# Optimization experiments

Measured on AMD Instinct MI355X. Metric: run time of the kernel, lower is better.

The kernel has to match this reference:

```python
import jax, jax.numpy as jnp
import numpy as np

B = 8        # graphs per batch
VG = 20000   # vertices per graph
K = 128      # eigenvectors per graph
D = 128      # channels (C_inout)
V = B * VG


def setup_inputs() -> dict:
    key = jax.random.key(0)
    kx, km, ke, kv, kt = jax.random.split(key, 5)
    x = jax.random.normal(kx, (V, D), dtype=jnp.float32)
    # lumped (diagonal) mass, positive
    mass = jax.random.uniform(km, (V,), dtype=jnp.float32, minval=0.5, maxval=1.5)
    # per-graph nonnegative eigenvalues, sorted within each graph, stacked to (B*K,)
    evals = jnp.sort(jax.random.uniform(ke, (B, K), dtype=jnp.float32) * 10.0, axis=1).reshape(-1)
    # eigenbasis, roughly mass-orthonormal scale
    evecs = jax.random.normal(kv, (V, K), dtype=jnp.float32) / np.sqrt(VG)
    # learned per-channel diffusion times, positive
    diffusion_time = jax.random.uniform(kt, (D,), dtype=jnp.float32, minval=0.01, maxval=0.2)
    batch = jnp.repeat(jnp.arange(B, dtype=jnp.int32), VG)
    return {"x": x, "mass": mass, "evals": evals, "evecs": evecs,
            "diffusion_time": diffusion_time, "batch": batch, "bs": B}


def reference(x, mass, evals, evecs, diffusion_time, batch, bs):
    Vtot, Dc = x.shape
    neig = evals.shape[0] // bs
    vg = Vtot // bs  # equal-sized graphs -> ragged grouped matmul == batched matmul
    t = jnp.maximum(diffusion_time, 1e-8)  # torch clamp(min=1e-8)
    xb = x.reshape(bs, vg, Dc)            # (B, Vg, D)
    eb = evecs.reshape(bs, vg, neig)      # (B, Vg, K)
    mb = mass.reshape(bs, vg)             # (B, Vg) diagonal mass
    # to_basis: basis^T @ (M x) per graph -> (B, K, D)
    x_spec = jnp.einsum('bvk,bvd->bkd', eb * mb[..., None], xb)
    # spectral diffusion coefficients exp(-lambda * t_c): (B, K, D)
    coefs = jnp.exp(-evals.reshape(bs, neig)[..., None] * t[None, None, :])
    # from_basis: evecs @ (coefs * x_spec) per graph -> (B, Vg, D)
    x_diffuse = jnp.einsum('bvk,bkd->bvd', eb, coefs * x_spec)
    return x_diffuse.reshape(Vtot, Dc)
```

## Files before the change

### kernel.cpp

```cpp
#include <hip/hip_runtime.h>

#define BGR 8
#define VG  20000
#define NK  128
#define ND  128

typedef float f32x4 __attribute__((ext_vector_type(4)));
typedef short bf16x8 __attribute__((ext_vector_type(8)));

__device__ __forceinline__ unsigned cvtpk(float a, float b) {
    unsigned r;
    asm("v_cvt_pk_bf16_f32 %0, %1, %2" : "=v"(r) : "v"(a), "v"(b));
    return r;
}

__device__ __forceinline__ short bf16r(float f) {
    union { float f; unsigned u; } c; c.f = f;
    unsigned r = (c.u + 0x7FFFu + ((c.u >> 16) & 1u)) >> 16;
    return (short)r;
}

#define VC  160
#define S1  40
#define NCH (VG / VC)

__global__ __launch_bounds__(256) void k_spec(const float* __restrict__ x,
                                              const float* __restrict__ mass,
                                              const float* __restrict__ evecs,
                                              float* __restrict__ scr) {
    const int bid   = blockIdx.x;
    const int g     = bid & 7;
    const int chunk = bid >> 3;
    const int v0    = chunk * VC;

    const float* xg = x     + (size_t)g * VG * ND;
    const float* eg = evecs + (size_t)g * VG * NK;
    const float* mg = mass  + (size_t)g * VG;

    __shared__ short Et[NK * S1];
    __shared__ short Xt[ND * S1];

    const int tid = threadIdx.x;
    const int l   = tid & 63;
    const int w   = tid >> 6;
    const int lo  = l & 15, hi = l >> 4;
    const int r0  = (w & 1) * 64, c0 = (w >> 1) * 64;

    const int cc = l;
    const int oc = w;

    float eA[8], eB[8], xA[8], xB[8], mm[8];

    auto loadr = [&](int r) {
        const int vb = v0 + r * 32 + oc * 8;
#pragma unroll
        for (int q = 0; q < 8; ++q) {
            const size_t re = (size_t)(vb + q) * NK;
            const size_t rx = (size_t)(vb + q) * ND;
            eA[q] = eg[re + cc];  eB[q] = eg[re + cc + 64];
            xA[q] = xg[rx + cc];  xB[q] = xg[rx + cc + 64];
            mm[q] = mg[vb + q];
        }
    };

    f32x4 acc[4][4] = {};
    loadr(0);

#pragma unroll
    for (int r = 0; r < VC / 32; ++r) {
        uint4 u;
        u.x = cvtpk(eA[0], eA[1]); u.y = cvtpk(eA[2], eA[3]);
        u.z = cvtpk(eA[4], eA[5]); u.w = cvtpk(eA[6], eA[7]);
        *(uint4*)(Et + cc * S1 + oc * 8) = u;
        u.x = cvtpk(eB[0], eB[1]); u.y = cvtpk(eB[2], eB[3]);
        u.z = cvtpk(eB[4], eB[5]); u.w = cvtpk(eB[6], eB[7]);
        *(uint4*)(Et + (cc + 64) * S1 + oc * 8) = u;
        u.x = cvtpk(xA[0] * mm[0], xA[1] * mm[1]); u.y = cvtpk(xA[2] * mm[2], xA[3] * mm[3]);
        u.z = cvtpk(xA[4] * mm[4], xA[5] * mm[5]); u.w = cvtpk(xA[6] * mm[6], xA[7] * mm[7]);
        *(uint4*)(Xt + cc * S1 + oc * 8) = u;
        u.x = cvtpk(xB[0] * mm[0], xB[1] * mm[1]); u.y = cvtpk(xB[2] * mm[2], xB[3] * mm[3]);
        u.z = cvtpk(xB[4] * mm[4], xB[5] * mm[5]); u.w = cvtpk(xB[6] * mm[6], xB[7] * mm[7]);
        *(uint4*)(Xt + (cc + 64) * S1 + oc * 8) = u;

        if (r + 1 < VC / 32) loadr(r + 1);
        __syncthreads();

        bf16x8 ax[4], be[4];
#pragma unroll
        for (int i = 0; i < 4; ++i)
            ax[i] = *(const bf16x8*)(Xt + (r0 + 16 * i + lo) * S1 + hi * 8);
#pragma unroll
        for (int j = 0; j < 4; ++j)
            be[j] = *(const bf16x8*)(Et + (c0 + 16 * j + lo) * S1 + hi * 8);
#pragma unroll
        for (int i = 0; i < 4; ++i)
#pragma unroll
            for (int j = 0; j < 4; ++j)
                acc[i][j] = __builtin_amdgcn_mfma_f32_16x16x32_bf16(ax[i], be[j], acc[i][j], 0, 0, 0);
        __syncthreads();
    }

    float* sg = scr + (size_t)bid * ND * NK;
#pragma unroll
    for (int i = 0; i < 4; ++i)
#pragma unroll
        for (int j = 0; j < 4; ++j)
#pragma unroll
            for (int t = 0; t < 4; ++t) {
                const int dd = r0 + 16 * i + hi * 4 + t;
                const int kk = c0 + 16 * j + lo;
                sg[dd * NK + kk] = acc[i][j][t];
            }
}

__global__ __launch_bounds__(256) void k_coef(const float* __restrict__ scr,
                                              const float* __restrict__ evals,
                                              const float* __restrict__ dt,
                                              short* __restrict__ Yt) {
    const int q   = blockIdx.x * 256 + threadIdx.x;
    const int g   = q >> 14;
    const int rem = q & 16383;
    const int d   = rem >> 7;
    const int k   = rem & 127;
    const float* p = scr + (size_t)g * ND * NK + rem;
    float s = 0.f;
#pragma unroll 25
    for (int c = 0; c < NCH; ++c)
        s += p[(size_t)c * 8 * ND * NK];
    const float t = fmaxf(dt[d], 1e-8f);
    Yt[q] = bf16r(__expf(-evals[g * NK + k] * t) * s);
}

#define TV  64
#define NT  ((VG + TV - 1) / TV)
#define NSL 64

__global__ __launch_bounds__(256) void k_out(const float* __restrict__ evecs,
                                             const short* __restrict__ Yt,
                                             float* __restrict__ out) {
    const int bid  = blockIdx.x;
    const int g    = bid & 7;
    const int slot = bid >> 3;

    const float* eg = evecs + (size_t)g * VG * NK;
    float*       og = out   + (size_t)g * VG * ND;
    const short* yg = Yt    + (size_t)g * ND * NK;

    __shared__ short Bs[128 * 128];
    __shared__ short As[2][TV * 128];

    const int tid = threadIdx.x;

#pragma unroll
    for (int it = 0; it < 8; ++it) {
        const int s16 = it * 256 + tid;
        const int rr  = s16 >> 4, gq = s16 & 15;
        *(uint4*)(Bs + rr * 128 + ((gq ^ (rr & 7)) << 3)) =
            *(const uint4*)(yg + s16 * 8);
    }

    const int vrow = tid >> 2;
    const int q4   = tid & 3;

    float4 ld[8];
    auto load_tile = [&](int t) {
        const int tv0  = t * TV;
        const int rows = (VG - tv0 < TV) ? (VG - tv0) : TV;
        const int vc   = vrow < rows ? vrow : rows - 1;
        const float* src = eg + (size_t)(tv0 + vc) * NK + q4 * 32;
#pragma unroll
        for (int f = 0; f < 8; ++f) ld[f] = *(const float4*)(src + 4 * f);
    };
    auto write_tile = [&](int buf) {
        short* A = As[buf];
#pragma unroll
        for (int h = 0; h < 4; ++h) {
            uint4 u;
            u.x = cvtpk(ld[2 * h].x, ld[2 * h].y);
            u.y = cvtpk(ld[2 * h].z, ld[2 * h].w);
            u.z = cvtpk(ld[2 * h + 1].x, ld[2 * h + 1].y);
            u.w = cvtpk(ld[2 * h + 1].z, ld[2 * h + 1].w);
            const int g8 = q4 * 4 + h;
            *(uint4*)(A + vrow * 128 + ((g8 ^ (vrow & 7)) << 3)) = u;
        }
    };

    const int l  = tid & 63;
    const int w  = tid >> 6;
    const int lo = l & 15, hi = l >> 4;
    const int r0 = (w & 1) * 32, c0 = (w >> 1) * 64;

    int t = slot;
    load_tile(t);
    write_tile(0);
    int cur = 0;

    for (; t < NT; t += NSL) {
        const int tn = t + NSL;
        if (tn < NT) load_tile(tn);
        __syncthreads();

        f32x4 acc[2][4] = {};
        const short* A = As[cur];
#pragma unroll
        for (int ks = 0; ks < 4; ++ks) {
            bf16x8 af[2], bv[4];
#pragma unroll
            for (int i = 0; i < 2; ++i) {
                const int R = r0 + 16 * i + lo;
                af[i] = *(const bf16x8*)(A + R * 128 + ((((ks << 2) + hi) ^ (R & 7)) << 3));
            }
#pragma unroll
            for (int j = 0; j < 4; ++j) {
                const int Dd = c0 + 16 * j + lo;
                bv[j] = *(const bf16x8*)(Bs + Dd * 128 + ((((ks << 2) + hi) ^ (Dd & 7)) << 3));
            }
#pragma unroll
            for (int i = 0; i < 2; ++i)
#pragma unroll
                for (int j = 0; j < 4; ++j)
                    acc[i][j] = __builtin_amdgcn_mfma_f32_16x16x32_bf16(af[i], bv[j], acc[i][j], 0, 0, 0);
        }

        const int tv0  = t * TV;
        const int rows = (VG - tv0 < TV) ? (VG - tv0) : TV;
#pragma unroll
        for (int i = 0; i < 2; ++i)
#pragma unroll
            for (int j = 0; j < 4; ++j)
#pragma unroll
                for (int u = 0; u < 4; ++u) {
                    const int vv = r0 + 16 * i + hi * 4 + u;
                    if (vv < rows)
                        og[(size_t)(tv0 + vv) * ND + c0 + 16 * j + lo] = acc[i][j][u];
                }

        if (tn < NT) write_tile(cur ^ 1);
        cur ^= 1;
    }
}

extern "C" void kernel_launch(void* const* d_in, const int* in_sizes, int n_in,
                              void* d_out, int out_size, void* d_ws, size_t ws_size,
                              hipStream_t stream) {
    const float* x     = (const float*)d_in[0];
    const float* mass  = (const float*)d_in[1];
    const float* evals = (const float*)d_in[2];
    const float* evecs = (const float*)d_in[3];
    const float* dt    = (const float*)d_in[4];
    float* out = (float*)d_out;

    float* scr = out;
    short* Yt  = (short*)d_ws;

    k_spec<<<NCH * BGR, 256, 0, stream>>>(x, mass, evecs, scr);
    k_coef<<<(BGR * ND * NK) / 256, 256, 0, stream>>>(scr, evals, dt, Yt);
    k_out<<<NSL * BGR, 256, 0, stream>>>(evecs, Yt, out);
}
```

Baseline: 252.4 us.

## Deepen load pipelining in spec and output kernels, widen loads, swizzle LDS

```diff
diff --git a/kernel.cpp b/kernel.cpp
--- a/kernel.cpp
+++ b/kernel.cpp
@@ -39,66 +39,80 @@
 
     __shared__ short Et[NK * S1];
     __shared__ short Xt[ND * S1];
+    __shared__ float Ms[VC];
 
     const int tid = threadIdx.x;
     const int l   = tid & 63;
     const int w   = tid >> 6;
     const int lo  = l & 15, hi = l >> 4;
     const int r0  = (w & 1) * 64, c0 = (w >> 1) * 64;
-
-    const int cc = l;
-    const int oc = w;
-
-    float eA[8], eB[8], xA[8], xB[8], mm[8];
-
-    auto loadr = [&](int r) {
-        const int vb = v0 + r * 32 + oc * 8;
-#pragma unroll
-        for (int q = 0; q < 8; ++q) {
-            const size_t re = (size_t)(vb + q) * NK;
-            const size_t rx = (size_t)(vb + q) * ND;
-            eA[q] = eg[re + cc];  eB[q] = eg[re + cc + 64];
-            xA[q] = xg[rx + cc];  xB[q] = xg[rx + cc + 64];
-            mm[q] = mg[vb + q];
-        }
-    };
+    const int oc  = w;
+    const int C0  = 2 * l;
+    const int sw  = ((oc ^ ((l >> 2) & 3)) << 3);
+
+    if (tid < VC) Ms[tid] = mg[v0 + tid];
+
+    float2 e0[8], x0[8], e1[8], x1[8];
+
+#define ISSUE_SPEC(EB, XB, r) do {                                          \
+    const int vb_ = v0 + (r) * 32 + oc * 8;                                 \
+    _Pragma("unroll")                                                       \
+    for (int q = 0; q < 8; ++q) {                                           \
+        EB[q] = *(const float2*)(eg + (size_t)(vb_ + q) * NK + C0);         \
+        XB[q] = *(const float2*)(xg + (size_t)(vb_ + q) * ND + C0);         \
+    } } while (0)
+
+#define PACK_SPEC(EB, XB, r) do {                                           \
+    const int mb_ = (r) * 32 + oc * 8;                                      \
+    float m_[8];                                                            \
+    _Pragma("unroll")                                                       \
+    for (int q = 0; q < 8; ++q) m_[q] = Ms[mb_ + q];                        \
+    uint4 u_;                                                               \
+    u_.x = cvtpk(EB[0].x, EB[1].x); u_.y = cvtpk(EB[2].x, EB[3].x);         \
+    u_.z = cvtpk(EB[4].x, EB[5].x); u_.w = cvtpk(EB[6].x, EB[7].x);         \
+    *(uint4*)(Et + C0 * S1 + sw) = u_;                                      \
+    u_.x = cvtpk(EB[0].y, EB[1].y); u_.y = cvtpk(EB[2].y, EB[3].y);         \
+    u_.z = cvtpk(EB[4].y, EB[5].y); u_.w = cvtpk(EB[6].y, EB[7].y);         \
+    *(uint4*)(Et + (C0 + 1) * S1 + sw) = u_;                                \
+    u_.x = cvtpk(XB[0].x * m_[0], XB[1].x * m_[1]);                         \
+    u_.y = cvtpk(XB[2].x * m_[2], XB[3].x * m_[3]);                         \
+    u_.z = cvtpk(XB[4].x * m_[4], XB[5].x * m_[5]);                         \
+    u_.w = cvtpk(XB[6].x * m_[6], XB[7].x * m_[7]);                         \
+    *(uint4*)(Xt + C0 * S1 + sw) = u_;                                      \
+    u_.x = cvtpk(XB[0].y * m_[0], XB[1].y * m_[1]);                         \
+    u_.y = cvtpk(XB[2].y * m_[2], XB[3].y * m_[3]);                         \
+    u_.z = cvtpk(XB[4].y * m_[4], XB[5].y * m_[5]);                         \
+    u_.w = cvtpk(XB[6].y * m_[6], XB[7].y * m_[7]);                         \
+    *(uint4*)(Xt + (C0 + 1) * S1 + sw) = u_;                                \
+    } while (0)
+
+#define MFMA_SPEC() do {                                                    \
+    bf16x8 ax_[4], be_[4];                                                  \
+    _Pragma("unroll")                                                       \
+    for (int i = 0; i < 4; ++i) {                                           \
+        const int R_ = r0 + 16 * i + lo;                                    \
+        ax_[i] = *(const bf16x8*)(Xt + R_ * S1 + ((hi ^ ((R_ >> 3) & 3)) << 3)); } \
+    _Pragma("unroll")                                                       \
+    for (int j = 0; j < 4; ++j) {                                           \
+        const int R_ = c0 + 16 * j + lo;                                    \
+        be_[j] = *(const bf16x8*)(Et + R_ * S1 + ((hi ^ ((R_ >> 3) & 3)) << 3)); } \
+    _Pragma("unroll")                                                       \
+    for (int i = 0; i < 4; ++i)                                             \
+    _Pragma("unroll")                                                       \
+    for (int j = 0; j < 4; ++j)                                             \
+        acc[i][j] = __builtin_amdgcn_mfma_f32_16x16x32_bf16(ax_[i], be_[j], acc[i][j], 0, 0, 0); \
+    } while (0)
 
     f32x4 acc[4][4] = {};
-    loadr(0);
-
-#pragma unroll
-    for (int r = 0; r < VC / 32; ++r) {
-        uint4 u;
-        u.x = cvtpk(eA[0], eA[1]); u.y = cvtpk(eA[2], eA[3]);
-        u.z = cvtpk(eA[4], eA[5]); u.w = cvtpk(eA[6], eA[7]);
-        *(uint4*)(Et + cc * S1 + oc * 8) = u;
-        u.x = cvtpk(eB[0], eB[1]); u.y = cvtpk(eB[2], eB[3]);
-        u.z = cvtpk(eB[4], eB[5]); u.w = cvtpk(eB[6], eB[7]);
-        *(uint4*)(Et + (cc + 64) * S1 + oc * 8) = u;
-        u.x = cvtpk(xA[0] * mm[0], xA[1] * mm[1]); u.y = cvtpk(xA[2] * mm[2], xA[3] * mm[3]);
-        u.z = cvtpk(xA[4] * mm[4], xA[5] * mm[5]); u.w = cvtpk(xA[6] * mm[6], xA[7] * mm[7]);
-        *(uint4*)(Xt + cc * S1 + oc * 8) = u;
-        u.x = cvtpk(xB[0] * mm[0], xB[1] * mm[1]); u.y = cvtpk(xB[2] * mm[2], xB[3] * mm[3]);
-        u.z = cvtpk(xB[4] * mm[4], xB[5] * mm[5]); u.w = cvtpk(xB[6] * mm[6], xB[7] * mm[7]);
-        *(uint4*)(Xt + (cc + 64) * S1 + oc * 8) = u;
-
-        if (r + 1 < VC / 32) loadr(r + 1);
-        __syncthreads();
-
-        bf16x8 ax[4], be[4];
-#pragma unroll
-        for (int i = 0; i < 4; ++i)
-            ax[i] = *(const bf16x8*)(Xt + (r0 + 16 * i + lo) * S1 + hi * 8);
-#pragma unroll
-        for (int j = 0; j < 4; ++j)
-            be[j] = *(const bf16x8*)(Et + (c0 + 16 * j + lo) * S1 + hi * 8);
-#pragma unroll
-        for (int i = 0; i < 4; ++i)
-#pragma unroll
-            for (int j = 0; j < 4; ++j)
-                acc[i][j] = __builtin_amdgcn_mfma_f32_16x16x32_bf16(ax[i], be[j], acc[i][j], 0, 0, 0);
-        __syncthreads();
-    }
+
+    ISSUE_SPEC(e0, x0, 0);
+    __syncthreads();
+
+    ISSUE_SPEC(e1, x1, 1); PACK_SPEC(e0, x0, 0); __syncthreads(); MFMA_SPEC(); __syncthreads();
+    ISSUE_SPEC(e0, x0, 2); PACK_SPEC(e1, x1, 1); __syncthreads(); MFMA_SPEC(); __syncthreads();
+    ISSUE_SPEC(e1, x1, 3); PACK_SPEC(e0, x0, 2); __syncthreads(); MFMA_SPEC(); __syncthreads();
+    ISSUE_SPEC(e0, x0, 4); PACK_SPEC(e1, x1, 3); __syncthreads(); MFMA_SPEC(); __syncthreads();
+    PACK_SPEC(e0, x0, 4); __syncthreads(); MFMA_SPEC();
 
     float* sg = scr + (size_t)bid * ND * NK;
 #pragma unroll
@@ -111,15 +125,18 @@
                 const int kk = c0 + 16 * j + lo;
                 sg[dd * NK + kk] = acc[i][j][t];
             }
+#undef ISSUE_SPEC
+#undef PACK_SPEC
+#undef MFMA_SPEC
 }
 
 __global__ __launch_bounds__(256) void k_coef(const float* __restrict__ scr,
                                               const float* __restrict__ evals,
                                               const float* __restrict__ dt,
                                               short* __restrict__ Yt) {
-    const int q   = blockIdx.x * 256 + threadIdx.x;
-    const int g   = q >> 14;
-    const int rem = q & 16383;
+    const int bid = blockIdx.x;
+    const int g   = bid & 7;
+    const int rem = (bid >> 3) * 256 + threadIdx.x;
     const int d   = rem >> 7;
     const int k   = rem & 127;
     const float* p = scr + (size_t)g * ND * NK + rem;
@@ -128,19 +145,21 @@
     for (int c = 0; c < NCH; ++c)
         s += p[(size_t)c * 8 * ND * NK];
     const float t = fmaxf(dt[d], 1e-8f);
-    Yt[q] = bf16r(__expf(-evals[g * NK + k] * t) * s);
-}
-
-#define TV  64
-#define NT  ((VG + TV - 1) / TV)
-#define NSL 64
+    Yt[(size_t)g * ND * NK + rem] = bf16r(__expf(-evals[g * NK + k] * t) * s);
+}
+
+#define TV    64
+#define TPB   5
+#define VSPAN (TV * TPB)
+#define NBLK  ((VG + VSPAN - 1) / VSPAN)
 
 __global__ __launch_bounds__(256) void k_out(const float* __restrict__ evecs,
                                              const short* __restrict__ Yt,
                                              float* __restrict__ out) {
-    const int bid  = blockIdx.x;
-    const int g    = bid & 7;
-    const int slot = bid >> 3;
+    const int bid    = blockIdx.x;
+    const int g      = bid & 7;
+    const int slot   = bid >> 3;
+    const int v_base = slot * VSPAN;
 
     const float* eg = evecs + (size_t)g * VG * NK;
     float*       og = out   + (size_t)g * VG * ND;
@@ -149,95 +168,98 @@
     __shared__ short Bs[128 * 128];
     __shared__ short As[2][TV * 128];
 
-    const int tid = threadIdx.x;
-
+    const int tid  = threadIdx.x;
+    const int vrow = tid >> 2;
+    const int q4   = tid & 3;
+
+    float4 ldA[8], ldB[8];
+
+#define ISSUE_OUT(BUF, t) do {                                              \
+    const int tv0_ = v_base + (t) * TV;                                     \
+    if (tv0_ < VG) {                                                        \
+        const int rows_ = (VG - tv0_ < TV) ? (VG - tv0_) : TV;              \
+        const int vc_   = vrow < rows_ ? vrow : rows_ - 1;                  \
+        const float* s_ = eg + (size_t)(tv0_ + vc_) * NK + q4 * 32;         \
+        _Pragma("unroll")                                                   \
+        for (int f = 0; f < 8; ++f) BUF[f] = *(const float4*)(s_ + 4 * f);  \
+    } } while (0)
+
+#define WRITE_OUT(BUF, t) do {                                              \
+    if (v_base + (t) * TV < VG) {                                           \
+        short* A_ = As[(t) & 1];                                            \
+        _Pragma("unroll")                                                   \
+        for (int h = 0; h < 4; ++h) {                                       \
+            uint4 u_;                                                       \
+            u_.x = cvtpk(BUF[2 * h].x, BUF[2 * h].y);                       \
+            u_.y = cvtpk(BUF[2 * h].z, BUF[2 * h].w);                       \
+            u_.z = cvtpk(BUF[2 * h + 1].x, BUF[2 * h + 1].y);               \
+            u_.w = cvtpk(BUF[2 * h + 1].z, BUF[2 * h + 1].w);               \
+            const int g8_ = q4 * 4 + h;                                     \
+            *(uint4*)(A_ + vrow * 128 + ((g8_ ^ (vrow & 7)) << 3)) = u_;    \
+        } } } while (0)
+
+    uint4 bq[8];
+#pragma unroll
+    for (int it = 0; it < 8; ++it)
+        bq[it] = *(const uint4*)(yg + (it * 256 + tid) * 8);
+    ISSUE_OUT(ldA, 0);
+    ISSUE_OUT(ldB, 1);
 #pragma unroll
     for (int it = 0; it < 8; ++it) {
         const int s16 = it * 256 + tid;
         const int rr  = s16 >> 4, gq = s16 & 15;
-        *(uint4*)(Bs + rr * 128 + ((gq ^ (rr & 7)) << 3)) =
-            *(const uint4*)(yg + s16 * 8);
+        *(uint4*)(Bs + rr * 128 + ((gq ^ (rr & 7)) << 3)) = bq[it];
     }
-
-    const int vrow = tid >> 2;
-    const int q4   = tid & 3;
-
-    float4 ld[8];
-    auto load_tile = [&](int t) {
-        const int tv0  = t * TV;
-        const int rows = (VG - tv0 < TV) ? (VG - tv0) : TV;
-        const int vc   = vrow < rows ? vrow : rows - 1;
-        const float* src = eg + (size_t)(tv0 + vc) * NK + q4 * 32;
-#pragma unroll
-        for (int f = 0; f < 8; ++f) ld[f] = *(const float4*)(src + 4 * f);
-    };
-    auto write_tile = [&](int buf) {
-        short* A = As[buf];
-#pragma unroll
-        for (int h = 0; h < 4; ++h) {
-            uint4 u;
-            u.x = cvtpk(ld[2 * h].x, ld[2 * h].y);
-            u.y = cvtpk(ld[2 * h].z, ld[2 * h].w);
-            u.z = cvtpk(ld[2 * h + 1].x, ld[2 * h + 1].y);
-            u.w = cvtpk(ld[2 * h + 1].z, ld[2 * h + 1].w);
-            const int g8 = q4 * 4 + h;
-            *(uint4*)(A + vrow * 128 + ((g8 ^ (vrow & 7)) << 3)) = u;
-        }
-    };
+    WRITE_OUT(ldA, 0);
+    __syncthreads();
 
     const int l  = tid & 63;
     const int w  = tid >> 6;
     const int lo = l & 15, hi = l >> 4;
     const int r0 = (w & 1) * 32, c0 = (w >> 1) * 64;
 
-    int t = slot;
-    load_tile(t);
-    write_tile(0);
-    int cur = 0;
-
-    for (; t < NT; t += NSL) {
-        const int tn = t + NSL;
-        if (tn < NT) load_tile(tn);
-        __syncthreads();
-
-        f32x4 acc[2][4] = {};
-        const short* A = As[cur];
-#pragma unroll
-        for (int ks = 0; ks < 4; ++ks) {
-            bf16x8 af[2], bv[4];
-#pragma unroll
-            for (int i = 0; i < 2; ++i) {
-                const int R = r0 + 16 * i + lo;
-                af[i] = *(const bf16x8*)(A + R * 128 + ((((ks << 2) + hi) ^ (R & 7)) << 3));
-            }
-#pragma unroll
-            for (int j = 0; j < 4; ++j) {
-                const int Dd = c0 + 16 * j + lo;
-                bv[j] = *(const bf16x8*)(Bs + Dd * 128 + ((((ks << 2) + hi) ^ (Dd & 7)) << 3));
-            }
-#pragma unroll
-            for (int i = 0; i < 2; ++i)
-#pragma unroll
-                for (int j = 0; j < 4; ++j)
-                    acc[i][j] = __builtin_amdgcn_mfma_f32_16x16x32_bf16(af[i], bv[j], acc[i][j], 0, 0, 0);
-        }
-
-        const int tv0  = t * TV;
-        const int rows = (VG - tv0 < TV) ? (VG - tv0) : TV;
-#pragma unroll
-        for (int i = 0; i < 2; ++i)
-#pragma unroll
-            for (int j = 0; j < 4; ++j)
-#pragma unroll
-                for (int u = 0; u < 4; ++u) {
-                    const int vv = r0 + 16 * i + hi * 4 + u;
-                    if (vv < rows)
-                        og[(size_t)(tv0 + vv) * ND + c0 + 16 * j + lo] = acc[i][j][u];
-                }
-
-        if (tn < NT) write_tile(cur ^ 1);
-        cur ^= 1;
-    }
+#define MFMA_OUT(t) do {                                                    \
+    const int tv0_ = v_base + (t) * TV;                                     \
+    if (tv0_ < VG) {                                                        \
+        const int rows_ = (VG - tv0_ < TV) ? (VG - tv0_) : TV;              \
+        const short* A_ = As[(t) & 1];                                      \
+        f32x4 acc[2][4] = {};                                               \
+        _Pragma("unroll")                                                   \
+        for (int ks = 0; ks < 4; ++ks) {                                    \
+            bf16x8 af_[2], bv_[4];                                          \
+            _Pragma("unroll")                                               \
+            for (int i = 0; i < 2; ++i) {                                   \
+                const int R_ = r0 + 16 * i + lo;                            \
+                af_[i] = *(const bf16x8*)(A_ + R_ * 128 + ((((ks << 2) + hi) ^ (R_ & 7)) << 3)); } \
+            _Pragma("unroll")                                               \
+            for (int j = 0; j < 4; ++j) {                                   \
+                const int D_ = c0 + 16 * j + lo;                            \
+                bv_[j] = *(const bf16x8*)(Bs + D_ * 128 + ((((ks << 2) + hi) ^ (D_ & 7)) << 3)); } \
+            _Pragma("unroll")                                               \
+            for (int i = 0; i < 2; ++i)                                     \
+            _Pragma("unroll")                                               \
+            for (int j = 0; j < 4; ++j)                                     \
+                acc[i][j] = __builtin_amdgcn_mfma_f32_16x16x32_bf16(af_[i], bv_[j], acc[i][j], 0, 0, 0); \
+        }                                                                   \
+        _Pragma("unroll")                                                   \
+        for (int i = 0; i < 2; ++i)                                         \
+        _Pragma("unroll")                                                   \
+        for (int j = 0; j < 4; ++j)                                         \
+        _Pragma("unroll")                                                   \
+        for (int u = 0; u < 4; ++u) {                                       \
+            const int vv_ = r0 + 16 * i + hi * 4 + u;                       \
+            if (vv_ < rows_)                                                \
+                og[(size_t)(tv0_ + vv_) * ND + c0 + 16 * j + lo] = acc[i][j][u]; \
+        } } } while (0)
+
+    ISSUE_OUT(ldA, 2); MFMA_OUT(0); WRITE_OUT(ldB, 1); __syncthreads();
+    ISSUE_OUT(ldB, 3); MFMA_OUT(1); WRITE_OUT(ldA, 2); __syncthreads();
+    ISSUE_OUT(ldA, 4); MFMA_OUT(2); WRITE_OUT(ldB, 3); __syncthreads();
+                       MFMA_OUT(3); WRITE_OUT(ldA, 4); __syncthreads();
+                       MFMA_OUT(4);
+#undef ISSUE_OUT
+#undef WRITE_OUT
+#undef MFMA_OUT
 }
 
 extern "C" void kernel_launch(void* const* d_in, const int* in_sizes, int n_in,
@@ -255,5 +277,5 @@
 
     k_spec<<<NCH * BGR, 256, 0, stream>>>(x, mass, evecs, scr);
     k_coef<<<(BGR * ND * NK) / 256, 256, 0, stream>>>(scr, evals, dt, Yt);
-    k_out<<<NSL * BGR, 256, 0, stream>>>(evecs, Yt, out);
-}
+    k_out<<<NBLK * BGR, 256, 0, stream>>>(evecs, Yt, out);
+}
```

Result: no change. 251.5 us (-0.3%).

## Load MFMA fragments directly from global memory, drop LDS staging in both GEMMs

Applied to the files above, without the earlier changes.

```diff
diff --git a/kernel.cpp b/kernel.cpp
--- a/kernel.cpp
+++ b/kernel.cpp
@@ -20,9 +20,8 @@
     return (short)r;
 }
 
-#define VC  160
-#define S1  40
-#define NCH (VG / VC)
+#define VC  320
+#define NCH ((VG + VC - 1) / VC)
 
 __global__ __launch_bounds__(256) void k_spec(const float* __restrict__ x,
                                               const float* __restrict__ mass,
@@ -32,13 +31,12 @@
     const int g     = bid & 7;
     const int chunk = bid >> 3;
     const int v0    = chunk * VC;
+    const int nv    = (VG - v0 < VC) ? (VG - v0) : VC;
+    const int rounds = nv >> 5;
 
     const float* xg = x     + (size_t)g * VG * ND;
     const float* eg = evecs + (size_t)g * VG * NK;
     const float* mg = mass  + (size_t)g * VG;
-
-    __shared__ short Et[NK * S1];
-    __shared__ short Xt[ND * S1];
 
     const int tid = threadIdx.x;
     const int l   = tid & 63;
@@ -46,58 +44,44 @@
     const int lo  = l & 15, hi = l >> 4;
     const int r0  = (w & 1) * 64, c0 = (w >> 1) * 64;
 
-    const int cc = l;
-    const int oc = w;
-
-    float eA[8], eB[8], xA[8], xB[8], mm[8];
-
-    auto loadr = [&](int r) {
-        const int vb = v0 + r * 32 + oc * 8;
-#pragma unroll
-        for (int q = 0; q < 8; ++q) {
-            const size_t re = (size_t)(vb + q) * NK;
-            const size_t rx = (size_t)(vb + q) * ND;
-            eA[q] = eg[re + cc];  eB[q] = eg[re + cc + 64];
-            xA[q] = xg[rx + cc];  xB[q] = xg[rx + cc + 64];
-            mm[q] = mg[vb + q];
+    const float* ax = xg + (size_t)(v0 + hi * 8) * ND + r0 + lo;
+    const float* be = eg + (size_t)(v0 + hi * 8) * NK + c0 + lo;
+    const float* mp = mg + v0 + hi * 8;
+
+    f32x4 acc[4][4] = {};
+
+#pragma unroll 1
+    for (int r = 0; r < rounds; ++r) {
+        float mv[8], xa[4][8], eb[4][8];
+#pragma unroll
+        for (int j = 0; j < 8; ++j) mv[j] = mp[j];
+#pragma unroll
+        for (int j = 0; j < 8; ++j)
+#pragma unroll
+            for (int i = 0; i < 4; ++i) {
+                xa[i][j] = ax[j * ND + i * 16];
+                eb[i][j] = be[j * NK + i * 16];
+            }
+
+        union { uint4 u; bf16x8 v; } pa[4], pb[4];
+#pragma unroll
+        for (int i = 0; i < 4; ++i) {
+            pa[i].u.x = cvtpk(xa[i][0] * mv[0], xa[i][1] * mv[1]);
+            pa[i].u.y = cvtpk(xa[i][2] * mv[2], xa[i][3] * mv[3]);
+            pa[i].u.z = cvtpk(xa[i][4] * mv[4], xa[i][5] * mv[5]);
+            pa[i].u.w = cvtpk(xa[i][6] * mv[6], xa[i][7] * mv[7]);
+            pb[i].u.x = cvtpk(eb[i][0], eb[i][1]);
+            pb[i].u.y = cvtpk(eb[i][2], eb[i][3]);
+            pb[i].u.z = cvtpk(eb[i][4], eb[i][5]);
+            pb[i].u.w = cvtpk(eb[i][6], eb[i][7]);
         }
-    };
-
-    f32x4 acc[4][4] = {};
-    loadr(0);
-
-#pragma unroll
-    for (int r = 0; r < VC / 32; ++r) {
-        uint4 u;
-        u.x = cvtpk(eA[0], eA[1]); u.y = cvtpk(eA[2], eA[3]);
-        u.z = cvtpk(eA[4], eA[5]); u.w = cvtpk(eA[6], eA[7]);
-        *(uint4*)(Et + cc * S1 + oc * 8) = u;
-        u.x = cvtpk(eB[0], eB[1]); u.y = cvtpk(eB[2], eB[3]);
-        u.z = cvtpk(eB[4], eB[5]); u.w = cvtpk(eB[6], eB[7]);
-        *(uint4*)(Et + (cc + 64) * S1 + oc * 8) = u;
-        u.x = cvtpk(xA[0] * mm[0], xA[1] * mm[1]); u.y = cvtpk(xA[2] * mm[2], xA[3] * mm[3]);
-        u.z = cvtpk(xA[4] * mm[4], xA[5] * mm[5]); u.w = cvtpk(xA[6] * mm[6], xA[7] * mm[7]);
-        *(uint4*)(Xt + cc * S1 + oc * 8) = u;
-        u.x = cvtpk(xB[0] * mm[0], xB[1] * mm[1]); u.y = cvtpk(xB[2] * mm[2], xB[3] * mm[3]);
-        u.z = cvtpk(xB[4] * mm[4], xB[5] * mm[5]); u.w = cvtpk(xB[6] * mm[6], xB[7] * mm[7]);
-        *(uint4*)(Xt + (cc + 64) * S1 + oc * 8) = u;
-
-        if (r + 1 < VC / 32) loadr(r + 1);
-        __syncthreads();
-
-        bf16x8 ax[4], be[4];
 #pragma unroll
         for (int i = 0; i < 4; ++i)
-            ax[i] = *(const bf16x8*)(Xt + (r0 + 16 * i + lo) * S1 + hi * 8);
-#pragma unroll
-        for (int j = 0; j < 4; ++j)
-            be[j] = *(const bf16x8*)(Et + (c0 + 16 * j + lo) * S1 + hi * 8);
-#pragma unroll
-        for (int i = 0; i < 4; ++i)
 #pragma unroll
             for (int j = 0; j < 4; ++j)
-                acc[i][j] = __builtin_amdgcn_mfma_f32_16x16x32_bf16(ax[i], be[j], acc[i][j], 0, 0, 0);
-        __syncthreads();
+                acc[i][j] = __builtin_amdgcn_mfma_f32_16x16x32_bf16(pa[i].v, pb[j].v, acc[i][j], 0, 0, 0);
+
+        ax += 32 * ND; be += 32 * NK; mp += 32;
     }
 
     float* sg = scr + (size_t)bid * ND * NK;
@@ -117,113 +101,88 @@
                                               const float* __restrict__ evals,
                                               const float* __restrict__ dt,
                                               short* __restrict__ Yt) {
-    const int q   = blockIdx.x * 256 + threadIdx.x;
-    const int g   = q >> 14;
-    const int rem = q & 16383;
+    const int bid = blockIdx.x;
+    const int g   = bid & 7;
+    const int rem = (bid >> 3) * 256 + threadIdx.x;
     const int d   = rem >> 7;
     const int k   = rem & 127;
     const float* p = scr + (size_t)g * ND * NK + rem;
     float s = 0.f;
-#pragma unroll 25
+#pragma unroll
     for (int c = 0; c < NCH; ++c)
         s += p[(size_t)c * 8 * ND * NK];
     const float t = fmaxf(dt[d], 1e-8f);
-    Yt[q] = bf16r(__expf(-evals[g * NK + k] * t) * s);
-}
-
-#define TV  64
-#define NT  ((VG + TV - 1) / TV)
-#define NSL 64
+    Yt[(size_t)g * ND * NK + rem] = bf16r(__expf(-evals[g * NK + k] * t) * s);
+}
+
+#define TV    64
+#define TPB   5
+#define VSPAN (TV * TPB)
+#define NBLK  ((VG + VSPAN - 1) / VSPAN)
 
 __global__ __launch_bounds__(256) void k_out(const float* __restrict__ evecs,
                                              const short* __restrict__ Yt,
                                              float* __restrict__ out) {
-    const int bid  = blockIdx.x;
-    const int g    = bid & 7;
-    const int slot = bid >> 3;
+    const int bid    = blockIdx.x;
+    const int g      = bid & 7;
+    const int slot   = bid >> 3;
+    const int v_base = slot * VSPAN;
 
     const float* eg = evecs + (size_t)g * VG * NK;
     float*       og = out   + (size_t)g * VG * ND;
     const short* yg = Yt    + (size_t)g * ND * NK;
 
-    __shared__ short Bs[128 * 128];
-    __shared__ short As[2][TV * 128];
-
     const int tid = threadIdx.x;
-
-#pragma unroll
-    for (int it = 0; it < 8; ++it) {
-        const int s16 = it * 256 + tid;
-        const int rr  = s16 >> 4, gq = s16 & 15;
-        *(uint4*)(Bs + rr * 128 + ((gq ^ (rr & 7)) << 3)) =
-            *(const uint4*)(yg + s16 * 8);
-    }
-
-    const int vrow = tid >> 2;
-    const int q4   = tid & 3;
-
-    float4 ld[8];
-    auto load_tile = [&](int t) {
-        const int tv0  = t * TV;
+    const int l   = tid & 63;
+    const int w   = tid >> 6;
+    const int lo  = l & 15, hi = l >> 4;
+    const int r0  = (w & 1) * 32, c0 = (w >> 1) * 64;
+
+    bf16x8 bv[4][4];
+#pragma unroll
+    for (int j = 0; j < 4; ++j)
+#pragma unroll
+        for (int ks = 0; ks < 4; ++ks)
+            bv[j][ks] = *(const bf16x8*)(yg + (c0 + 16 * j + lo) * NK + ks * 32 + hi * 8);
+
+#pragma unroll 1
+    for (int t = 0; t < TPB; ++t) {
+        const int tv0 = v_base + t * TV;
+        if (tv0 >= VG) break;
         const int rows = (VG - tv0 < TV) ? (VG - tv0) : TV;
-        const int vc   = vrow < rows ? vrow : rows - 1;
-        const float* src = eg + (size_t)(tv0 + vc) * NK + q4 * 32;
-#pragma unroll
-        for (int f = 0; f < 8; ++f) ld[f] = *(const float4*)(src + 4 * f);
-    };
-    auto write_tile = [&](int buf) {
-        short* A = As[buf];
-#pragma unroll
-        for (int h = 0; h < 4; ++h) {
-            uint4 u;
-            u.x = cvtpk(ld[2 * h].x, ld[2 * h].y);
-            u.y = cvtpk(ld[2 * h].z, ld[2 * h].w);
-            u.z = cvtpk(ld[2 * h + 1].x, ld[2 * h + 1].y);
-            u.w = cvtpk(ld[2 * h + 1].z, ld[2 * h + 1].w);
-            const int g8 = q4 * 4 + h;
-            *(uint4*)(A + vrow * 128 + ((g8 ^ (vrow & 7)) << 3)) = u;
+
+        float4 fa[2][4][2];
+#pragma unroll
+        for (int i = 0; i < 2; ++i) {
+            const int R  = r0 + 16 * i + lo;
+            const int Rc = R < rows ? R : rows - 1;
+            const float* ap = eg + (size_t)(tv0 + Rc) * NK + hi * 8;
+#pragma unroll
+            for (int ks = 0; ks < 4; ++ks) {
+                fa[i][ks][0] = *(const float4*)(ap + ks * 32);
+                fa[i][ks][1] = *(const float4*)(ap + ks * 32 + 4);
+            }
         }
-    };
-
-    const int l  = tid & 63;
-    const int w  = tid >> 6;
-    const int lo = l & 15, hi = l >> 4;
-    const int r0 = (w & 1) * 32, c0 = (w >> 1) * 64;
-
-    int t = slot;
-    load_tile(t);
-    write_tile(0);
-    int cur = 0;
-
-    for (; t < NT; t += NSL) {
-        const int tn = t + NSL;
-        if (tn < NT) load_tile(tn);
-        __syncthreads();
+        union { uint4 u; bf16x8 v; } af[2][4];
+#pragma unroll
+        for (int i = 0; i < 2; ++i)
+#pragma unroll
+            for (int ks = 0; ks < 4; ++ks) {
+                af[i][ks].u.x = cvtpk(fa[i][ks][0].x, fa[i][ks][0].y);
+                af[i][ks].u.y = cvtpk(fa[i][ks][0].z, fa[i][ks][0].w);
+                af[i][ks].u.z = cvtpk(fa[i][ks][1].x, fa[i][ks][1].y);
+                af[i][ks].u.w = cvtpk(fa[i][ks][1].z, fa[i][ks][1].w);
+            }
 
         f32x4 acc[2][4] = {};
-        const short* A = As[cur];
-#pragma unroll
-        for (int ks = 0; ks < 4; ++ks) {
-            bf16x8 af[2], bv[4];
-#pragma unroll
-            for (int i = 0; i < 2; ++i) {
-                const int R = r0 + 16 * i + lo;
-                af[i] = *(const bf16x8*)(A + R * 128 + ((((ks << 2) + hi) ^ (R & 7)) << 3));
-            }
-#pragma unroll
-            for (int j = 0; j < 4; ++j) {
-                const int Dd = c0 + 16 * j + lo;
-                bv[j] = *(const bf16x8*)(Bs + Dd * 128 + ((((ks << 2) + hi) ^ (Dd & 7)) << 3));
-            }
+#pragma unroll
+        for (int ks = 0; ks < 4; ++ks)
 #pragma unroll
             for (int i = 0; i < 2; ++i)
 #pragma unroll
                 for (int j = 0; j < 4; ++j)
-                    acc[i][j] = __builtin_amdgcn_mfma_f32_16x16x32_bf16(af[i], bv[j], acc[i][j], 0, 0, 0);
-        }
-
-        const int tv0  = t * TV;
-        const int rows = (VG - tv0 < TV) ? (VG - tv0) : TV;
+                    acc[i][j] = __builtin_amdgcn_mfma_f32_16x16x32_bf16(af[i][ks].v, bv[j][ks], acc[i][j], 0, 0, 0);
+
 #pragma unroll
         for (int i = 0; i < 2; ++i)
 #pragma unroll
@@ -234,9 +193,6 @@
                     if (vv < rows)
                         og[(size_t)(tv0 + vv) * ND + c0 + 16 * j + lo] = acc[i][j][u];
                 }
-
-        if (tn < NT) write_tile(cur ^ 1);
-        cur ^= 1;
     }
 }
 
@@ -255,5 +211,5 @@
 
     k_spec<<<NCH * BGR, 256, 0, stream>>>(x, mass, evecs, scr);
     k_coef<<<(BGR * ND * NK) / 256, 256, 0, stream>>>(scr, evals, dt, Yt);
-    k_out<<<NSL * BGR, 256, 0, stream>>>(evecs, Yt, out);
-}
+    k_out<<<NBLK * BGR, 256, 0, stream>>>(evecs, Yt, out);
+}
```

New measurement: 262.5 us. +4.0%, slower.
